# Optimization experiments

Measured on AMD Instinct MI355X. Metric: run time of the kernel, lower is better.

## Reference

```python
import jax, jax.numpy as jnp
import numpy as np

COMMITMENT_COST = 0.25


def setup_inputs() -> dict:
    key = jax.random.key(0)
    k1, k2 = jax.random.split(key)
    inputs = jax.random.normal(k1, (8, 1024, 512), dtype=jnp.float32)
    codebook = jax.random.normal(k2, (8192, 512), dtype=jnp.float32)
    return {"inputs": inputs, "codebook": codebook}


def reference(inputs, codebook):
    B, S, D = inputs.shape
    flat = inputs.reshape(-1, D)  # [N, D]
    distances = (
        jnp.sum(flat * flat, axis=1, keepdims=True)
        + jnp.sum(codebook * codebook, axis=1)
        - 2.0 * flat @ codebook.T
    )
    encoding_indices = jnp.argmin(distances, axis=1)  # [N] int
    min_distances = jnp.min(distances, axis=1)  # [N]
    quantized = codebook[encoding_indices].reshape(inputs.shape)  # [B,S,D]
    # straight-through estimator
    quantized_st = inputs + jax.lax.stop_gradient(quantized - inputs)
    # mse losses with reduction='sum'; .detach() -> stop_gradient
    loss_vq = jnp.sum((quantized - jax.lax.stop_gradient(inputs)) ** 2)
    loss_commit = jnp.sum((inputs - jax.lax.stop_gradient(quantized)) ** 2)
    # non-EMA branch: loss = commitment_cost * loss_commit + loss_vq
    loss = loss_commit * COMMITMENT_COST + loss_vq
    return (
        quantized_st,
        loss,
        encoding_indices.reshape(B, S),
        min_distances.reshape(B, S),
        loss_commit,
    )
```

## Files before the change

kernel.cpp:

```cpp
#include <hip/hip_runtime.h>

typedef __attribute__((ext_vector_type(8)))  short short8;
typedef __attribute__((ext_vector_type(16))) float f32x16;
typedef unsigned short ushort_t;
typedef unsigned int uint32;

#define NROWS 8192
#define NCODE 8192
#define DIM   512

#define OUT_Q      0
#define OUT_LOSS   4194304
#define OUT_IDX    4194305
#define OUT_MIND   4202497
#define OUT_COMMIT 4210689

#define WS_ENORM  0
#define WS_PMIN   8192
#define WS_PIDX   73728
#define WS_LPART  147456
#define WS_BHI    150528
#define WS_BLO    2247680

__device__ inline uint32 bf16_rne(float f) {
    uint32 u = __float_as_uint(f);
    return (u + 0x7FFFu + ((u >> 16) & 1u)) >> 16;
}

__device__ inline void gload16(const ushort_t* g, ushort_t* l) {
    __builtin_amdgcn_global_load_lds(
        (const __attribute__((address_space(1))) void*)g,
        (__attribute__((address_space(3))) void*)l, 16, 0, 0);
}

__global__ __launch_bounds__(256) void conv_kernel(const float* __restrict__ x,
                                                   const float* __restrict__ cb,
                                                   ushort_t* __restrict__ ahi,
                                                   ushort_t* __restrict__ alo,
                                                   ushort_t* __restrict__ bhi,
                                                   ushort_t* __restrict__ blo,
                                                   float* __restrict__ enorm) {
    int gid  = blockIdx.x * 256 + threadIdx.x;
    bool isA = gid < 524288;
    int g    = isA ? gid : gid - 524288;
    int row  = g >> 6;
    int lane = g & 63;
    int k0   = lane * 8;
    const float* src = (isA ? x : cb) + (size_t)row * DIM + k0;
    float v[8];
    *(float4*)&v[0] = *(const float4*)src;
    *(float4*)&v[4] = *(const float4*)(src + 4);
    float s = 0.0f;
    uint32 h[8], l[8];
    #pragma unroll
    for (int i = 0; i < 8; ++i) {
        s += v[i] * v[i];
        h[i] = bf16_rne(v[i]);
        float hf = __uint_as_float(h[i] << 16);
        l[i] = bf16_rne(v[i] - hf);
    }
    int tile = (row >> 7) * 16 + (k0 >> 5);
    int rp = row & 127, kp = k0 & 31;
    int c  = (rp >> 5) * 2 + (kp >> 4);
    int L  = (rp & 31) + (((kp >> 3) & 1) << 5);
    size_t off = (size_t)tile * 4096 + c * 512 + L * 8;
    uint4 ph, pl;
    ph.x = h[0] | (h[1] << 16); ph.y = h[2] | (h[3] << 16);
    ph.z = h[4] | (h[5] << 16); ph.w = h[6] | (h[7] << 16);
    pl.x = l[0] | (l[1] << 16); pl.y = l[2] | (l[3] << 16);
    pl.z = l[4] | (l[5] << 16); pl.w = l[6] | (l[7] << 16);
    if (isA) {
        *(uint4*)(ahi + off) = ph;
        *(uint4*)(alo + off) = pl;
    } else {
        *(uint4*)(bhi + off) = ph;
        *(uint4*)(blo + off) = pl;
        #pragma unroll
        for (int o = 32; o > 0; o >>= 1) s += __shfl_down(s, o);
        if (lane == 0) enorm[row] = s;
    }
}

__global__ __launch_bounds__(256, 2) void vq_mfma_kernel(
        const ushort_t* __restrict__ ahi, const ushort_t* __restrict__ alo,
        const ushort_t* __restrict__ bhi, const ushort_t* __restrict__ blo,
        const float* __restrict__ enorm,
        float* __restrict__ pmin, int* __restrict__ pidx) {
    __shared__ __align__(16) ushort_t smem[32768];

    const int tid  = threadIdx.x;
    const int wave = tid >> 6, lane = tid & 63;
    const int l31  = lane & 31, half = lane >> 5;
    const int q  = blockIdx.x;
    const int bx = (q & 7) * 8 + (q >> 6);
    const int by = (q >> 3) & 7;
    const int wrow = (wave >> 1) * 64;
    const int wcol = (wave & 1) * 64;
    const int so = wave * 512 + lane * 8;

    f32x16 acc[2][2];
    #pragma unroll
    for (int i = 0; i < 2; ++i)
        #pragma unroll
        for (int j = 0; j < 2; ++j)
            #pragma unroll
            for (int r = 0; r < 16; ++r) acc[i][j][r] = 0.0f;

    float bestd[32];
    int   besti[32];
    #pragma unroll
    for (int i = 0; i < 32; ++i) { bestd[i] = 3.4e38f; besti[i] = 0x7FFFFFFF; }

    auto stage = [&](int n) {
        const int kb = n & 15;
        const int ctile = by * 8 + (n >> 4);
        const size_t at = (size_t)(bx * 16 + kb) * 4096;
        const size_t bt = (size_t)(ctile * 16 + kb) * 4096;
        ushort_t* S = smem + (n & 1) * 16384;
        gload16(ahi + at + so,        S + so);
        gload16(ahi + at + 2048 + so, S + 2048 + so);
        gload16(alo + at + so,        S + 4096 + so);
        gload16(alo + at + 2048 + so, S + 6144 + so);
        gload16(bhi + bt + so,        S + 8192 + so);
        gload16(bhi + bt + 2048 + so, S + 10240 + so);
        gload16(blo + bt + so,        S + 12288 + so);
        gload16(blo + bt + 2048 + so, S + 14336 + so);
    };

    stage(0);

    for (int n = 0; n < 128; ++n) {
        __syncthreads();
        if (n + 1 < 128) stage(n + 1);

        ushort_t* S = smem + (n & 1) * 16384;
        #pragma unroll
        for (int k16 = 0; k16 < 2; ++k16) {
            short8 ah[2], al[2], bh[2], bl[2];
            #pragma unroll
            for (int ti = 0; ti < 2; ++ti) {
                int ca = ((wrow >> 5) + ti) * 2 + k16;
                ah[ti] = *(const short8*)&S[ca * 512 + lane * 8];
                al[ti] = *(const short8*)&S[4096 + ca * 512 + lane * 8];
            }
            #pragma unroll
            for (int tj = 0; tj < 2; ++tj) {
                int cb_ = ((wcol >> 5) + tj) * 2 + k16;
                bh[tj] = *(const short8*)&S[8192 + cb_ * 512 + lane * 8];
                bl[tj] = *(const short8*)&S[12288 + cb_ * 512 + lane * 8];
            }
            #pragma unroll
            for (int ti = 0; ti < 2; ++ti)
                #pragma unroll
                for (int tj = 0; tj < 2; ++tj) {
                    acc[ti][tj] = __builtin_amdgcn_mfma_f32_32x32x16_bf16(
                        ah[ti], bh[tj], acc[ti][tj], 0, 0, 0);
                    acc[ti][tj] = __builtin_amdgcn_mfma_f32_32x32x16_bf16(
                        ah[ti], bl[tj], acc[ti][tj], 0, 0, 0);
                    acc[ti][tj] = __builtin_amdgcn_mfma_f32_32x32x16_bf16(
                        al[ti], bh[tj], acc[ti][tj], 0, 0, 0);
                }
        }

        if ((n & 15) == 15) {
            const int ct = n >> 4;
            const int colbase = by * 1024 + ct * 128 + wcol;
            #pragma unroll
            for (int tj = 0; tj < 2; ++tj) {
                const int ci = colbase + tj * 32 + l31;
                const float en = enorm[ci];
                #pragma unroll
                for (int ti = 0; ti < 2; ++ti)
                    #pragma unroll
                    for (int reg = 0; reg < 16; ++reg) {
                        float d = en - 2.0f * acc[ti][tj][reg];
                        int s = ti * 16 + reg;
                        if (d < bestd[s]) { bestd[s] = d; besti[s] = ci; }
                    }
            }
            #pragma unroll
            for (int i = 0; i < 2; ++i)
                #pragma unroll
                for (int j = 0; j < 2; ++j)
                    #pragma unroll
                    for (int r = 0; r < 16; ++r) acc[i][j][r] = 0.0f;
        }
    }

    float* rd = (float*)smem;
    int*   ri = (int*)smem + 8192;
    __syncthreads();
    const int slot = (wave & 1) * 32 + l31;
    #pragma unroll
    for (int ti = 0; ti < 2; ++ti)
        #pragma unroll
        for (int reg = 0; reg < 16; ++reg) {
            int row = wrow + ti * 32 + (reg & 3) + 8 * (reg >> 2) + 4 * half;
            rd[slot * 128 + row] = bestd[ti * 16 + reg];
            ri[slot * 128 + row] = besti[ti * 16 + reg];
        }
    __syncthreads();
    if (tid < 128) {
        float bd = rd[tid];
        int   bi = ri[tid];
        #pragma unroll 8
        for (int t = 1; t < 64; ++t) {
            float d = rd[t * 128 + tid];
            int  ii = ri[t * 128 + tid];
            if (d < bd || (d == bd && ii < bi)) { bd = d; bi = ii; }
        }
        pmin[(size_t)(bx * 128 + tid) * 8 + by] = bd;
        pidx[(size_t)(bx * 128 + tid) * 8 + by] = bi;
    }
}

__global__ __launch_bounds__(256) void finish_kernel(const float* __restrict__ x,
                                                     const float* __restrict__ cb,
                                                     const float* __restrict__ pmin,
                                                     const int* __restrict__ pidx,
                                                     float* __restrict__ out_idx,
                                                     float* __restrict__ qout,
                                                     float* __restrict__ out_mind,
                                                     float* __restrict__ lpart) {
    __shared__ float sred[4];
    int row  = blockIdx.x * 4 + (threadIdx.x >> 6);
    int lane = threadIdx.x & 63;

    float d = (lane < 8) ? pmin[(size_t)row * 8 + lane] : 3.4e38f;
    int  ii = (lane < 8) ? pidx[(size_t)row * 8 + lane] : 0x7FFFFFFF;
    #pragma unroll
    for (int o = 4; o > 0; o >>= 1) {
        float d2 = __shfl_down(d, o);
        int   i2 = __shfl_down(ii, o);
        if (d2 < d || (d2 == d && i2 < ii)) { d = d2; ii = i2; }
    }
    int idx = __shfl(ii, 0);
    if (lane == 0) out_idx[row] = (float)idx;

    const float4* e4 = (const float4*)(cb + (size_t)idx * DIM);
    const float4* x4 = (const float4*)(x + (size_t)row * DIM);
    float4* q4 = (float4*)(qout + (size_t)row * DIM);
    float s = 0.0f;
    #pragma unroll
    for (int u = 0; u < 2; ++u) {
        float4 e  = e4[lane + u * 64];
        float4 xv = x4[lane + u * 64];
        q4[lane + u * 64] = e;
        float dx = xv.x - e.x, dy = xv.y - e.y, dz = xv.z - e.z, dw = xv.w - e.w;
        s += dx * dx + dy * dy + dz * dz + dw * dw;
    }
    #pragma unroll
    for (int o = 32; o > 0; o >>= 1) s += __shfl_down(s, o);
    if (lane == 0) { sred[threadIdx.x >> 6] = s; out_mind[row] = s; }
    __syncthreads();
    if (threadIdx.x == 0) lpart[blockIdx.x] = sred[0] + sred[1] + sred[2] + sred[3];
}

__global__ __launch_bounds__(256) void loss_kernel(const float* __restrict__ lpart,
                                                   float* __restrict__ out_loss,
                                                   float* __restrict__ out_commit) {
    __shared__ float sm[256];
    float s = 0.0f;
    for (int i = threadIdx.x; i < 2048; i += 256) s += lpart[i];
    sm[threadIdx.x] = s;
    __syncthreads();
    #pragma unroll
    for (int o = 128; o > 0; o >>= 1) {
        if (threadIdx.x < o) sm[threadIdx.x] += sm[threadIdx.x + o];
        __syncthreads();
    }
    if (threadIdx.x == 0) {
        *out_commit = sm[0];
        *out_loss   = 1.25f * sm[0];
    }
}

extern "C" void kernel_launch(void* const* d_in, const int* in_sizes, int n_in,
                              void* d_out, int out_size, void* d_ws, size_t ws_size,
                              hipStream_t stream) {
    const float* x  = (const float*)d_in[0];
    const float* cb = (const float*)d_in[1];
    float* out = (float*)d_out;
    float* ws  = (float*)d_ws;

    ushort_t* ahi = (ushort_t*)d_out;
    ushort_t* alo = (ushort_t*)d_out + 4194304;
    ushort_t* bhi = (ushort_t*)(ws + WS_BHI);
    ushort_t* blo = (ushort_t*)(ws + WS_BLO);
    float* enorm = ws + WS_ENORM;
    float* pmin  = ws + WS_PMIN;
    int*   pidx  = (int*)(ws + WS_PIDX);
    float* lpart = ws + WS_LPART;

    conv_kernel<<<4096, 256, 0, stream>>>(x, cb, ahi, alo, bhi, blo, enorm);
    vq_mfma_kernel<<<512, 256, 0, stream>>>(ahi, alo, bhi, blo, enorm, pmin, pidx);
    finish_kernel<<<NROWS / 4, 256, 0, stream>>>(x, cb, pmin, pidx,
                                                 out + OUT_IDX, out + OUT_Q,
                                                 out + OUT_MIND, lpart);
    loss_kernel<<<1, 256, 0, stream>>>(lpart, out + OUT_LOSS, out + OUT_COMMIT);
}
```

Measured before the change: 274.8 us.

## Replace split-bf16 GEMM with single bf16 pass plus fp32 candidate refinement

The distance GEMM switches from a three-MFMA hi/lo split-bf16 scheme to a single bf16 pass. Each group of eight codebook columns is reduced to a quantized 16-bit min-distance entry in a per-row matrix. A refine kernel then takes every group within an error bound of the row minimum (derived from the row norm and the largest codebook norm) and recomputes the exact fp32 distances for those candidates to choose the argmin. This removes two thirds of the MFMA work and the lo-half conversions. In exchange it adds a min-matrix write/read, a serial candidate loop, and correctness that depends on the error bound and the fixed quantization offset and scale holding for the input distribution.

Measured after the change: 395.7 us. +44.0%, slower.

```diff
diff --git a/kernel.cpp b/kernel.cpp
--- a/kernel.cpp
+++ b/kernel.cpp
@@ -4,6 +4,7 @@
 typedef __attribute__((ext_vector_type(16))) float f32x16;
 typedef unsigned short ushort_t;
 typedef unsigned int uint32;
+typedef unsigned long long uint64;
 
 #define NROWS 8192
 #define NCODE 8192
@@ -16,11 +17,11 @@
 #define OUT_COMMIT 4210689
 
 #define WS_ENORM  0
-#define WS_PMIN   8192
-#define WS_PIDX   73728
+#define WS_XNORM  8192
+#define WS_ENMAX  16384
 #define WS_LPART  147456
 #define WS_BHI    150528
-#define WS_BLO    2247680
+#define WS_MINMAT 2247680
 
 __device__ inline uint32 bf16_rne(float f) {
     uint32 u = __float_as_uint(f);
@@ -36,9 +37,8 @@
 __global__ __launch_bounds__(256) void conv_kernel(const float* __restrict__ x,
                                                    const float* __restrict__ cb,
                                                    ushort_t* __restrict__ ahi,
-                                                   ushort_t* __restrict__ alo,
                                                    ushort_t* __restrict__ bhi,
-                                                   ushort_t* __restrict__ blo,
+                                                   float* __restrict__ xnorm,
                                                    float* __restrict__ enorm) {
     int gid  = blockIdx.x * 256 + threadIdx.x;
     bool isA = gid < 524288;
@@ -51,192 +51,182 @@
     *(float4*)&v[0] = *(const float4*)src;
     *(float4*)&v[4] = *(const float4*)(src + 4);
     float s = 0.0f;
-    uint32 h[8], l[8];
+    uint32 h[8];
     #pragma unroll
     for (int i = 0; i < 8; ++i) {
         s += v[i] * v[i];
         h[i] = bf16_rne(v[i]);
-        float hf = __uint_as_float(h[i] << 16);
-        l[i] = bf16_rne(v[i] - hf);
     }
     int tile = (row >> 7) * 16 + (k0 >> 5);
     int rp = row & 127, kp = k0 & 31;
     int c  = (rp >> 5) * 2 + (kp >> 4);
     int L  = (rp & 31) + (((kp >> 3) & 1) << 5);
     size_t off = (size_t)tile * 4096 + c * 512 + L * 8;
-    uint4 ph, pl;
+    uint4 ph;
     ph.x = h[0] | (h[1] << 16); ph.y = h[2] | (h[3] << 16);
     ph.z = h[4] | (h[5] << 16); ph.w = h[6] | (h[7] << 16);
-    pl.x = l[0] | (l[1] << 16); pl.y = l[2] | (l[3] << 16);
-    pl.z = l[4] | (l[5] << 16); pl.w = l[6] | (l[7] << 16);
-    if (isA) {
-        *(uint4*)(ahi + off) = ph;
-        *(uint4*)(alo + off) = pl;
-    } else {
-        *(uint4*)(bhi + off) = ph;
-        *(uint4*)(blo + off) = pl;
-        #pragma unroll
-        for (int o = 32; o > 0; o >>= 1) s += __shfl_down(s, o);
-        if (lane == 0) enorm[row] = s;
-    }
+    if (isA) *(uint4*)(ahi + off) = ph;
+    else     *(uint4*)(bhi + off) = ph;
+    #pragma unroll
+    for (int o = 32; o > 0; o >>= 1) s += __shfl_down(s, o);
+    if (lane == 0) { if (isA) xnorm[row] = s; else enorm[row] = s; }
+}
+
+__global__ __launch_bounds__(256) void prep_kernel(const float* __restrict__ enorm,
+                                                   float* __restrict__ enmax) {
+    __shared__ float sm[256];
+    float m = 0.0f;
+    for (int i = threadIdx.x; i < NCODE; i += 256) m = fmaxf(m, enorm[i]);
+    sm[threadIdx.x] = m;
+    __syncthreads();
+    #pragma unroll
+    for (int o = 128; o > 0; o >>= 1) {
+        if (threadIdx.x < o) sm[threadIdx.x] = fmaxf(sm[threadIdx.x], sm[threadIdx.x + o]);
+        __syncthreads();
+    }
+    if (threadIdx.x == 0) enmax[0] = sm[0];
 }
 
 __global__ __launch_bounds__(256, 2) void vq_mfma_kernel(
-        const ushort_t* __restrict__ ahi, const ushort_t* __restrict__ alo,
-        const ushort_t* __restrict__ bhi, const ushort_t* __restrict__ blo,
-        const float* __restrict__ enorm,
-        float* __restrict__ pmin, int* __restrict__ pidx) {
-    __shared__ __align__(16) ushort_t smem[32768];
+        const ushort_t* __restrict__ ahi, const ushort_t* __restrict__ bhi,
+        const float* __restrict__ enorm, ushort_t* __restrict__ minmat) {
+    __shared__ __align__(16) ushort_t smem[12288];
 
     const int tid  = threadIdx.x;
     const int wave = tid >> 6, lane = tid & 63;
     const int l31  = lane & 31, half = lane >> 5;
     const int q  = blockIdx.x;
-    const int bx = (q & 7) * 8 + (q >> 6);
-    const int by = (q >> 3) & 7;
-    const int wrow = (wave >> 1) * 64;
-    const int wcol = (wave & 1) * 64;
-    const int so = wave * 512 + lane * 8;
-
-    f32x16 acc[2][2];
+    const int bx = (q & 7) * 8 + (q >> 8);
+    const int by = (q >> 3) & 31;
+    const int wr = wave >> 1;
+    const int wc = wave & 1;
+
+    f32x16 acc[2][4];
     #pragma unroll
     for (int i = 0; i < 2; ++i)
         #pragma unroll
-        for (int j = 0; j < 2; ++j)
+        for (int j = 0; j < 4; ++j)
             #pragma unroll
             for (int r = 0; r < 16; ++r) acc[i][j][r] = 0.0f;
 
-    float bestd[32];
-    int   besti[32];
-    #pragma unroll
-    for (int i = 0; i < 32; ++i) { bestd[i] = 3.4e38f; besti[i] = 0x7FFFFFFF; }
-
     auto stage = [&](int n) {
-        const int kb = n & 15;
-        const int ctile = by * 8 + (n >> 4);
-        const size_t at = (size_t)(bx * 16 + kb) * 4096;
-        const size_t bt = (size_t)(ctile * 16 + kb) * 4096;
-        ushort_t* S = smem + (n & 1) * 16384;
-        gload16(ahi + at + so,        S + so);
-        gload16(ahi + at + 2048 + so, S + 2048 + so);
-        gload16(alo + at + so,        S + 4096 + so);
-        gload16(alo + at + 2048 + so, S + 6144 + so);
-        gload16(bhi + bt + so,        S + 8192 + so);
-        gload16(bhi + bt + 2048 + so, S + 10240 + so);
-        gload16(blo + bt + so,        S + 12288 + so);
-        gload16(blo + bt + 2048 + so, S + 14336 + so);
+        const int kc = n >> 1, k16 = n & 1;
+        ushort_t* S = smem + (n & 1) * 6144;
+        const int lo = (tid >> 6) * 1024 + (k16 << 9) + (tid & 63) * 8;
+        gload16(ahi + (((size_t)(bx * 16 + kc)) << 12) + lo, S + tid * 8);
+        gload16(bhi + (((size_t)((by * 2)     * 16 + kc)) << 12) + lo, S + 2048 + tid * 8);
+        gload16(bhi + (((size_t)((by * 2 + 1) * 16 + kc)) << 12) + lo, S + 4096 + tid * 8);
     };
 
     stage(0);
-
-    for (int n = 0; n < 128; ++n) {
+    #pragma unroll 2
+    for (int n = 0; n < 32; ++n) {
         __syncthreads();
-        if (n + 1 < 128) stage(n + 1);
-
-        ushort_t* S = smem + (n & 1) * 16384;
-        #pragma unroll
-        for (int k16 = 0; k16 < 2; ++k16) {
-            short8 ah[2], al[2], bh[2], bl[2];
-            #pragma unroll
-            for (int ti = 0; ti < 2; ++ti) {
-                int ca = ((wrow >> 5) + ti) * 2 + k16;
-                ah[ti] = *(const short8*)&S[ca * 512 + lane * 8];
-                al[ti] = *(const short8*)&S[4096 + ca * 512 + lane * 8];
+        if (n < 31) stage(n + 1);
+        const ushort_t* S = smem + (n & 1) * 6144;
+        short8 ah[2], bh[4];
+        #pragma unroll
+        for (int ti = 0; ti < 2; ++ti)
+            ah[ti] = *(const short8*)&S[(wr * 2 + ti) * 512 + lane * 8];
+        #pragma unroll
+        for (int tj = 0; tj < 4; ++tj)
+            bh[tj] = *(const short8*)&S[2048 + (wc * 4 + tj) * 512 + lane * 8];
+        __builtin_amdgcn_s_setprio(1);
+        #pragma unroll
+        for (int ti = 0; ti < 2; ++ti)
+            #pragma unroll
+            for (int tj = 0; tj < 4; ++tj)
+                acc[ti][tj] = __builtin_amdgcn_mfma_f32_32x32x16_bf16(
+                    ah[ti], bh[tj], acc[ti][tj], 0, 0, 0);
+        __builtin_amdgcn_s_setprio(0);
+    }
+
+    const int colbase = by * 256 + wc * 128;
+    #pragma unroll
+    for (int tj = 0; tj < 4; ++tj) {
+        const int ci = colbase + tj * 32 + l31;
+        const float en = enorm[ci];
+        #pragma unroll
+        for (int ti = 0; ti < 2; ++ti)
+            #pragma unroll
+            for (int r = 0; r < 16; ++r) {
+                float d  = en - 2.0f * acc[ti][tj][r];
+                float qf = fminf(fmaxf((d + 1536.0f) * 16.0f, 0.0f), 65535.0f);
+                qf = fminf(qf, __shfl_xor(qf, 1));
+                qf = fminf(qf, __shfl_xor(qf, 2));
+                qf = fminf(qf, __shfl_xor(qf, 4));
+                if ((l31 & 7) == 0) {
+                    int row = bx * 128 + wr * 64 + ti * 32
+                            + (r & 3) + 8 * (r >> 2) + 4 * half;
+                    int sub = (colbase >> 3) + tj * 4 + (l31 >> 3);
+                    minmat[(size_t)row * 1024 + sub] =
+                        (ushort_t)__float2uint_rn(qf);
+                }
             }
-            #pragma unroll
-            for (int tj = 0; tj < 2; ++tj) {
-                int cb_ = ((wcol >> 5) + tj) * 2 + k16;
-                bh[tj] = *(const short8*)&S[8192 + cb_ * 512 + lane * 8];
-                bl[tj] = *(const short8*)&S[12288 + cb_ * 512 + lane * 8];
+    }
+}
+
+__global__ __launch_bounds__(256) void refine_kernel(
+        const float* __restrict__ x, const float* __restrict__ cb,
+        const float* __restrict__ xnorm, const float* __restrict__ enorm,
+        const float* __restrict__ enmax, const ushort_t* __restrict__ minmat,
+        float* __restrict__ out_idx, float* __restrict__ qout,
+        float* __restrict__ out_mind, float* __restrict__ lpart) {
+    __shared__ float sred[4];
+    const int wave = threadIdx.x >> 6, lane = threadIdx.x & 63;
+    const int row  = blockIdx.x * 4 + wave;
+
+    const ushort_t* mrow = minmat + (size_t)row * 1024;
+    uint4 a0 = ((const uint4*)mrow)[lane * 2];
+    uint4 a1 = ((const uint4*)mrow)[lane * 2 + 1];
+    uint32 w[8] = {a0.x, a0.y, a0.z, a0.w, a1.x, a1.y, a1.z, a1.w};
+    uint32 mn = 0xFFFFu;
+    #pragma unroll
+    for (int i = 0; i < 8; ++i)
+        mn = min(mn, min(w[i] & 0xFFFFu, w[i] >> 16));
+    #pragma unroll
+    for (int o = 1; o < 64; o <<= 1) mn = min(mn, __shfl_xor(mn, o));
+
+    const float xn = xnorm[row];
+    const float T  = 0.0160f * sqrtf(xn * enmax[0]) + 0.2f;
+    const uint32 thr = mn + (uint32)(32.0f * T) + 3u;
+
+    float bestd = 3.4e38f;
+    int   besti = 0x7FFFFFFF;
+    const float* xr = x + (size_t)row * DIM;
+    #pragma unroll
+    for (int t = 0; t < 16; ++t) {
+        uint32 qv = (t & 1) ? (w[t >> 1] >> 16) : (w[t >> 1] & 0xFFFFu);
+        uint64 mask = __ballot(qv <= thr);
+        while (mask) {
+            int L = __builtin_ctzll(mask); mask &= mask - 1;
+            int sub = L * 16 + t;
+            int c   = sub * 8 + (lane >> 3);
+            int ks  = lane & 7;
+            const float4* e4 = (const float4*)(cb + (size_t)c * DIM) + ks * 16;
+            const float4* x4 = (const float4*)xr + ks * 16;
+            float dot = 0.0f;
+            #pragma unroll
+            for (int u = 0; u < 16; ++u) {
+                float4 e = e4[u]; float4 xv = x4[u];
+                dot += xv.x * e.x + xv.y * e.y + xv.z * e.z + xv.w * e.w;
             }
-            #pragma unroll
-            for (int ti = 0; ti < 2; ++ti)
-                #pragma unroll
-                for (int tj = 0; tj < 2; ++tj) {
-                    acc[ti][tj] = __builtin_amdgcn_mfma_f32_32x32x16_bf16(
-                        ah[ti], bh[tj], acc[ti][tj], 0, 0, 0);
-                    acc[ti][tj] = __builtin_amdgcn_mfma_f32_32x32x16_bf16(
-                        ah[ti], bl[tj], acc[ti][tj], 0, 0, 0);
-                    acc[ti][tj] = __builtin_amdgcn_mfma_f32_32x32x16_bf16(
-                        al[ti], bh[tj], acc[ti][tj], 0, 0, 0);
-                }
+            dot += __shfl_xor(dot, 1);
+            dot += __shfl_xor(dot, 2);
+            dot += __shfl_xor(dot, 4);
+            float d = xn + enorm[c] - 2.0f * dot;
+            #pragma unroll
+            for (int o = 8; o < 64; o <<= 1) {
+                float d2 = __shfl_xor(d, o);
+                int   c2 = __shfl_xor(c, o);
+                if (d2 < d || (d2 == d && c2 < c)) { d = d2; c = c2; }
+            }
+            if (d < bestd || (d == bestd && c < besti)) { bestd = d; besti = c; }
         }
-
-        if ((n & 15) == 15) {
-            const int ct = n >> 4;
-            const int colbase = by * 1024 + ct * 128 + wcol;
-            #pragma unroll
-            for (int tj = 0; tj < 2; ++tj) {
-                const int ci = colbase + tj * 32 + l31;
-                const float en = enorm[ci];
-                #pragma unroll
-                for (int ti = 0; ti < 2; ++ti)
-                    #pragma unroll
-                    for (int reg = 0; reg < 16; ++reg) {
-                        float d = en - 2.0f * acc[ti][tj][reg];
-                        int s = ti * 16 + reg;
-                        if (d < bestd[s]) { bestd[s] = d; besti[s] = ci; }
-                    }
-            }
-            #pragma unroll
-            for (int i = 0; i < 2; ++i)
-                #pragma unroll
-                for (int j = 0; j < 2; ++j)
-                    #pragma unroll
-                    for (int r = 0; r < 16; ++r) acc[i][j][r] = 0.0f;
-        }
-    }
-
-    float* rd = (float*)smem;
-    int*   ri = (int*)smem + 8192;
-    __syncthreads();
-    const int slot = (wave & 1) * 32 + l31;
-    #pragma unroll
-    for (int ti = 0; ti < 2; ++ti)
-        #pragma unroll
-        for (int reg = 0; reg < 16; ++reg) {
-            int row = wrow + ti * 32 + (reg & 3) + 8 * (reg >> 2) + 4 * half;
-            rd[slot * 128 + row] = bestd[ti * 16 + reg];
-            ri[slot * 128 + row] = besti[ti * 16 + reg];
-        }
-    __syncthreads();
-    if (tid < 128) {
-        float bd = rd[tid];
-        int   bi = ri[tid];
-        #pragma unroll 8
-        for (int t = 1; t < 64; ++t) {
-            float d = rd[t * 128 + tid];
-            int  ii = ri[t * 128 + tid];
-            if (d < bd || (d == bd && ii < bi)) { bd = d; bi = ii; }
-        }
-        pmin[(size_t)(bx * 128 + tid) * 8 + by] = bd;
-        pidx[(size_t)(bx * 128 + tid) * 8 + by] = bi;
-    }
-}
-
-__global__ __launch_bounds__(256) void finish_kernel(const float* __restrict__ x,
-                                                     const float* __restrict__ cb,
-                                                     const float* __restrict__ pmin,
-                                                     const int* __restrict__ pidx,
-                                                     float* __restrict__ out_idx,
-                                                     float* __restrict__ qout,
-                                                     float* __restrict__ out_mind,
-                                                     float* __restrict__ lpart) {
-    __shared__ float sred[4];
-    int row  = blockIdx.x * 4 + (threadIdx.x >> 6);
-    int lane = threadIdx.x & 63;
-
-    float d = (lane < 8) ? pmin[(size_t)row * 8 + lane] : 3.4e38f;
-    int  ii = (lane < 8) ? pidx[(size_t)row * 8 + lane] : 0x7FFFFFFF;
-    #pragma unroll
-    for (int o = 4; o > 0; o >>= 1) {
-        float d2 = __shfl_down(d, o);
-        int   i2 = __shfl_down(ii, o);
-        if (d2 < d || (d2 == d && i2 < ii)) { d = d2; ii = i2; }
-    }
-    int idx = __shfl(ii, 0);
+    }
+
+    int idx = besti;
     if (lane == 0) out_idx[row] = (float)idx;
-
     const float4* e4 = (const float4*)(cb + (size_t)idx * DIM);
     const float4* x4 = (const float4*)(x + (size_t)row * DIM);
     float4* q4 = (float4*)(qout + (size_t)row * DIM);
@@ -251,9 +241,10 @@
     }
     #pragma unroll
     for (int o = 32; o > 0; o >>= 1) s += __shfl_down(s, o);
-    if (lane == 0) { sred[threadIdx.x >> 6] = s; out_mind[row] = s; }
+    if (lane == 0) { sred[wave] = s; out_mind[row] = s; }
     __syncthreads();
-    if (threadIdx.x == 0) lpart[blockIdx.x] = sred[0] + sred[1] + sred[2] + sred[3];
+    if (threadIdx.x == 0)
+        lpart[blockIdx.x] = sred[0] + sred[1] + sred[2] + sred[3];
 }
 
 __global__ __launch_bounds__(256) void loss_kernel(const float* __restrict__ lpart,
@@ -283,19 +274,19 @@
     float* out = (float*)d_out;
     float* ws  = (float*)d_ws;
 
-    ushort_t* ahi = (ushort_t*)d_out;
-    ushort_t* alo = (ushort_t*)d_out + 4194304;
-    ushort_t* bhi = (ushort_t*)(ws + WS_BHI);
-    ushort_t* blo = (ushort_t*)(ws + WS_BLO);
+    ushort_t* ahi    = (ushort_t*)d_out;
+    ushort_t* bhi    = (ushort_t*)(ws + WS_BHI);
+    ushort_t* minmat = (ushort_t*)(ws + WS_MINMAT);
+    float* xnorm = ws + WS_XNORM;
     float* enorm = ws + WS_ENORM;
-    float* pmin  = ws + WS_PMIN;
-    int*   pidx  = (int*)(ws + WS_PIDX);
+    float* enmax = ws + WS_ENMAX;
     float* lpart = ws + WS_LPART;
 
-    conv_kernel<<<4096, 256, 0, stream>>>(x, cb, ahi, alo, bhi, blo, enorm);
-    vq_mfma_kernel<<<512, 256, 0, stream>>>(ahi, alo, bhi, blo, enorm, pmin, pidx);
-    finish_kernel<<<NROWS / 4, 256, 0, stream>>>(x, cb, pmin, pidx,
-                                                 out + OUT_IDX, out + OUT_Q,
-                                                 out + OUT_MIND, lpart);
+    conv_kernel<<<4096, 256, 0, stream>>>(x, cb, ahi, bhi, xnorm, enorm);
+    prep_kernel<<<1, 256, 0, stream>>>(enorm, enmax);
+    vq_mfma_kernel<<<2048, 256, 0, stream>>>(ahi, bhi, enorm, minmat);
+    refine_kernel<<<2048, 256, 0, stream>>>(x, cb, xnorm, enorm, enmax, minmat,
+                                            out + OUT_IDX, out + OUT_Q,
+                                            out + OUT_MIND, lpart);
     loss_kernel<<<1, 256, 0, stream>>>(lpart, out + OUT_LOSS, out + OUT_COMMIT);
 }
```
